# Performance work log

Hardware: AMD Instinct MI355X
Metric: run time of the kernel (lower is better)

The kernel has to match this reference:

```python
import jax, jax.numpy as jnp
import numpy as np

N_SRC, N_TGT, E = 50000, 10000, 150000
D_IN, D_OUT = 512, 512
N_ETYPES, N_NTYPES = 8, 4


def setup_inputs() -> dict:
    key = jax.random.key(0)
    ks = jax.random.split(key, 9)
    scale = 1.0 / np.sqrt(D_IN)
    return {
        "x_src": jax.random.normal(ks[0], (N_SRC, D_IN), jnp.float32),
        "x_target": jax.random.normal(ks[1], (N_TGT, D_IN), jnp.float32),
        "rel_W": jax.random.normal(ks[2], (N_ETYPES, D_IN, D_OUT), jnp.float32) * scale,
        "root_W": jax.random.normal(ks[3], (N_NTYPES, D_IN, D_OUT), jnp.float32) * scale,
        "root_b": jax.random.normal(ks[4], (N_NTYPES, D_OUT), jnp.float32) * scale,
        "edge_src": jax.random.randint(ks[5], (E,), 0, N_SRC, jnp.int64).astype(jnp.int32),
        "edge_dst": jax.random.randint(ks[6], (E,), 0, N_TGT, jnp.int64).astype(jnp.int32),
        "edge_type": jax.random.randint(ks[7], (E,), 0, N_ETYPES, jnp.int64).astype(jnp.int32),
        "target_node_type": jax.random.randint(ks[8], (N_TGT,), 0, N_NTYPES, jnp.int64).astype(jnp.int32),
    }


def reference(x_src, x_target, rel_W, root_W, root_b,
              edge_src, edge_dst, edge_type, target_node_type):
    T = rel_W.shape[0]
    n_tgt = x_target.shape[0]
    # Transform every source node under every relation (grouped GEMM),
    # then gather per edge: msg_e = W_{etype_e} @ x_src[src_e].
    h = jnp.einsum('ni,tio->tno', x_src, rel_W)          # [T, N_src, D_out]
    msg = h[edge_type, edge_src]                          # [E, D_out]
    # PyG aggr='mean' is applied per edge type then SUMMED across types:
    # segment-mean keyed by (dst, etype), empty segments contribute 0.
    seg = edge_dst * T + edge_type                        # [E]
    sums = jax.ops.segment_sum(msg, seg, num_segments=n_tgt * T)
    counts = jax.ops.segment_sum(jnp.ones((msg.shape[0],), msg.dtype), seg,
                                 num_segments=n_tgt * T)
    means = sums / jnp.maximum(counts, 1.0)[:, None]      # [N_tgt*T, D_out]
    out = means.reshape(n_tgt, T, -1).sum(axis=1)         # [N_tgt, D_out]
    # Per-node-type root linear (with bias), selected per target node.
    root = jnp.einsum('ni,tio->nto', x_target, root_W) + root_b[None]  # [N_tgt, NT, D_out]
    root_sel = jnp.take_along_axis(root, target_node_type[:, None, None], axis=1)[:, 0]
    return out + root_sel
```

## Files before the change

### kernel.cpp

```cpp
#include <hip/hip_runtime.h>
#include <hip/hip_bf16.h>

#define D 512
#define T_ETYPES 8
#define NT_TYPES 4
#define K_MAIN 4096
#define K_TOT 6144
#define SPLITS 4
#define KSPLIT 1536

typedef __attribute__((ext_vector_type(8))) short bf16x8;
typedef __attribute__((ext_vector_type(4))) float f32x4;

__device__ __forceinline__ unsigned short f2bf(float f) {
    union { float f; unsigned u; } u{f};
    unsigned r = u.u + 0x7FFF + ((u.u >> 16) & 1);
    return (unsigned short)(r >> 16);
}
__device__ __forceinline__ float bf2f(unsigned short h) {
    union { unsigned u; float f; } v{(unsigned)h << 16};
    return v.f;
}

__device__ __forceinline__ void gl16(const unsigned short* g, unsigned short* l) {
    __builtin_amdgcn_global_load_lds(
        (const __attribute__((address_space(1))) unsigned int*)g,
        (__attribute__((address_space(3))) unsigned int*)l,
        16, 0, 0);
}

__global__ void convert_weights(const float* __restrict__ relW,
                                const float* __restrict__ rootW,
                                unsigned short* __restrict__ WbT) {
    __shared__ float tile[32][33];
    int c0 = blockIdx.x * 32;
    int o0 = blockIdx.y * 32;
    int tid = threadIdx.x;
#pragma unroll
    for (int it = 0; it < 4; ++it) {
        int idx = it * 256 + tid;
        int oc = idx & 31, cc = idx >> 5;
        int c = c0 + cc, o = o0 + oc;
        float v = (c < K_MAIN) ? relW[(size_t)c * D + o]
                               : rootW[(size_t)(c - K_MAIN) * D + o];
        tile[cc][oc] = v;
    }
    __syncthreads();
#pragma unroll
    for (int it = 0; it < 4; ++it) {
        int idx = it * 256 + tid;
        int cc = idx & 31, oc = idx >> 5;
        WbT[(size_t)(o0 + oc) * K_TOT + (c0 + cc)] = f2bf(tile[cc][oc]);
    }
}

__global__ void hist_kernel(const int* __restrict__ edst, const int* __restrict__ etyp,
                            int* __restrict__ counts, int E) {
    int e = blockIdx.x * 256 + threadIdx.x;
    if (e < E) atomicAdd(&counts[edst[e] * T_ETYPES + etyp[e]], 1);
}

__global__ void scan1(const int* __restrict__ counts, int* __restrict__ partial,
                      int* __restrict__ blockSums, int n) {
    __shared__ int sh[256];
    int tid = threadIdx.x, i = blockIdx.x * 256 + tid;
    int c = (i < n) ? counts[i] : 0;
    int val = c;
    sh[tid] = val; __syncthreads();
#pragma unroll
    for (int off = 1; off < 256; off <<= 1) {
        int add = (tid >= off) ? sh[tid - off] : 0;
        __syncthreads();
        val += add; sh[tid] = val;
        __syncthreads();
    }
    if (i < n) partial[i] = val - c;
    if (tid == 255) blockSums[blockIdx.x] = val;
}

__global__ void scan2(int* __restrict__ blockSums, int nb) {
    __shared__ int sh[512];
    int tid = threadIdx.x;
    int c = (tid < nb) ? blockSums[tid] : 0;
    int val = c;
    sh[tid] = val; __syncthreads();
#pragma unroll
    for (int off = 1; off < 512; off <<= 1) {
        int add = (tid >= off) ? sh[tid - off] : 0;
        __syncthreads();
        val += add; sh[tid] = val;
        __syncthreads();
    }
    if (tid < nb) blockSums[tid] = val - c;
}

__global__ void scan3(const int* __restrict__ partial, const int* __restrict__ blockSums,
                      int* __restrict__ offsets, int* __restrict__ cursors, int n) {
    int i = blockIdx.x * 256 + threadIdx.x;
    if (i < n) {
        int v = partial[i] + blockSums[i >> 8];
        offsets[i] = v;
        cursors[i] = v;
    }
}

__global__ void scatter_kernel(const int* __restrict__ esrc, const int* __restrict__ edst,
                               const int* __restrict__ etyp, int* __restrict__ cursors,
                               int* __restrict__ perm, int E) {
    int e = blockIdx.x * 256 + threadIdx.x;
    if (e < E) {
        int seg = edst[e] * T_ETYPES + etyp[e];
        int pos = atomicAdd(&cursors[seg], 1);
        perm[pos] = esrc[e];
    }
}

__global__ void segmean(const float* __restrict__ x_src, const int* __restrict__ perm,
                        const int* __restrict__ offsets, const int* __restrict__ counts,
                        unsigned short* __restrict__ A, int nseg) {
    int seg = blockIdx.x * 4 + (threadIdx.x >> 6);
    if (seg >= nseg) return;
    int lane = threadIdx.x & 63;
    int beg = offsets[seg], cnt = counts[seg];
    float4 a0 = make_float4(0.f, 0.f, 0.f, 0.f);
    float4 a1 = make_float4(0.f, 0.f, 0.f, 0.f);
    for (int i = 0; i < cnt; ++i) {
        int s = perm[beg + i];
        const float4* p = reinterpret_cast<const float4*>(x_src + (size_t)s * D);
        float4 v0 = p[lane * 2], v1 = p[lane * 2 + 1];
        a0.x += v0.x; a0.y += v0.y; a0.z += v0.z; a0.w += v0.w;
        a1.x += v1.x; a1.y += v1.y; a1.z += v1.z; a1.w += v1.w;
    }
    float sc = (cnt > 0) ? 1.0f / (float)cnt : 0.0f;
    uint4 u;
    u.x = (unsigned)f2bf(a0.x * sc) | ((unsigned)f2bf(a0.y * sc) << 16);
    u.y = (unsigned)f2bf(a0.z * sc) | ((unsigned)f2bf(a0.w * sc) << 16);
    u.z = (unsigned)f2bf(a1.x * sc) | ((unsigned)f2bf(a1.y * sc) << 16);
    u.w = (unsigned)f2bf(a1.z * sc) | ((unsigned)f2bf(a1.w * sc) << 16);
    int dst = seg >> 3, t = seg & 7;
    *reinterpret_cast<uint4*>(A + (size_t)dst * K_TOT + t * D + lane * 8) = u;
}

__global__ void rootfill(const float* __restrict__ x_target, const int* __restrict__ tnt,
                         unsigned short* __restrict__ A, int M) {
    int n = blockIdx.x;
    int tid = threadIdx.x;
    int nt = tnt[n];
    int col = tid * 8;
    int g = col >> 9;
    uint4 u = make_uint4(0, 0, 0, 0);
    if (g == nt) {
        const float4* p = reinterpret_cast<const float4*>(x_target + (size_t)n * D + (col & 511));
        float4 v0 = p[0], v1 = p[1];
        u.x = (unsigned)f2bf(v0.x) | ((unsigned)f2bf(v0.y) << 16);
        u.y = (unsigned)f2bf(v0.z) | ((unsigned)f2bf(v0.w) << 16);
        u.z = (unsigned)f2bf(v1.x) | ((unsigned)f2bf(v1.y) << 16);
        u.w = (unsigned)f2bf(v1.z) | ((unsigned)f2bf(v1.w) << 16);
    }
    *reinterpret_cast<uint4*>(A + (size_t)n * K_TOT + K_MAIN + col) = u;
}

__global__ __launch_bounds__(256, 4)
void rgcn_gemm_sk(const unsigned short* __restrict__ A,
                  const unsigned short* __restrict__ WbT,
                  unsigned short* __restrict__ pbuf, int M, int MB) {
    __shared__ unsigned short As[128 * 32];
    __shared__ unsigned short Bs[128 * 32];
    const int tid = threadIdx.x;

    int d = blockIdx.x;
    int l = d;
    if ((gridDim.x & 7) == 0) {
        int cpx = gridDim.x >> 3;
        l = (d & 7) * cpx + (d >> 3);
    }
    const int nIdx = l & 3;
    const int mz = l >> 2;
    const int mIdx = mz % MB;
    const int zIdx = mz / MB;

    const int blockM = mIdx * 128;
    const int blockN = nIdx * 128;
    const int kBase = zIdx * KSPLIT;
    const int wid = tid >> 6, lane = tid & 63;
    const int wr = wid >> 1, wc = wid & 1;
    const int lr = lane & 15, lg = lane >> 4;

    f32x4 acc[4][4] = {};

    const int c0 = tid, c1 = 256 + tid;
    const unsigned short* Abase = A + (size_t)blockM * K_TOT + kBase;
    const unsigned short* Bbase = WbT + (size_t)blockN * K_TOT + kBase;

    for (int k0 = 0; k0 < KSPLIT; k0 += 32) {
        gl16(Abase + (size_t)(c0 >> 2) * K_TOT + k0 + (c0 & 3) * 8, &As[c0 * 8]);
        gl16(Abase + (size_t)(c1 >> 2) * K_TOT + k0 + (c1 & 3) * 8, &As[c1 * 8]);
        gl16(Bbase + (size_t)(c0 >> 2) * K_TOT + k0 + (c0 & 3) * 8, &Bs[c0 * 8]);
        gl16(Bbase + (size_t)(c1 >> 2) * K_TOT + k0 + (c1 & 3) * 8, &Bs[c1 * 8]);
        __syncthreads();

        bf16x8 a_frag[4], b_frag[4];
#pragma unroll
        for (int mi = 0; mi < 4; ++mi)
            a_frag[mi] = *reinterpret_cast<const bf16x8*>(&As[(wr * 64 + mi * 16 + lr) * 32 + lg * 8]);
#pragma unroll
        for (int ni = 0; ni < 4; ++ni)
            b_frag[ni] = *reinterpret_cast<const bf16x8*>(&Bs[(wc * 64 + ni * 16 + lr) * 32 + lg * 8]);
#pragma unroll
        for (int mi = 0; mi < 4; ++mi)
#pragma unroll
            for (int ni = 0; ni < 4; ++ni)
                acc[mi][ni] = __builtin_amdgcn_mfma_f32_16x16x32_bf16(a_frag[mi], b_frag[ni], acc[mi][ni], 0, 0, 0);
        __syncthreads();
    }

#pragma unroll
    for (int mi = 0; mi < 4; ++mi) {
#pragma unroll
        for (int r = 0; r < 4; ++r) {
            int row = blockM + wr * 64 + mi * 16 + lg * 4 + r;
            if (row < M) {
#pragma unroll
                for (int ni = 0; ni < 4; ++ni) {
                    int col = blockN + wc * 64 + ni * 16 + lr;
                    pbuf[((size_t)zIdx * M + row) * D + col] = f2bf(acc[mi][ni][r]);
                }
            }
        }
    }
}

__global__ void reduce_bias(const unsigned short* __restrict__ pbuf,
                            const int* __restrict__ tnt, const float* __restrict__ root_b,
                            float* __restrict__ out, int M) {
    int idx = blockIdx.x * 256 + threadIdx.x;
    if (idx >= M * (D / 8)) return;
    int row = idx >> 6;
    int col = (idx & 63) * 8;
    float s[8] = {0.f, 0.f, 0.f, 0.f, 0.f, 0.f, 0.f, 0.f};
#pragma unroll
    for (int sp = 0; sp < SPLITS; ++sp) {
        uint4 v = *reinterpret_cast<const uint4*>(pbuf + ((size_t)sp * M + row) * D + col);
        unsigned u[4] = {v.x, v.y, v.z, v.w};
#pragma unroll
        for (int j = 0; j < 4; ++j) {
            s[2 * j]     += bf2f((unsigned short)(u[j] & 0xFFFF));
            s[2 * j + 1] += bf2f((unsigned short)(u[j] >> 16));
        }
    }
    const float* b = root_b + (size_t)tnt[row] * D + col;
    float4 o0, o1;
    o0.x = s[0] + b[0]; o0.y = s[1] + b[1]; o0.z = s[2] + b[2]; o0.w = s[3] + b[3];
    o1.x = s[4] + b[4]; o1.y = s[5] + b[5]; o1.z = s[6] + b[6]; o1.w = s[7] + b[7];
    float* o = out + (size_t)row * D + col;
    *reinterpret_cast<float4*>(o) = o0;
    *reinterpret_cast<float4*>(o + 4) = o1;
}

extern "C" void kernel_launch(void* const* d_in, const int* in_sizes, int n_in,
                              void* d_out, int out_size, void* d_ws, size_t ws_size,
                              hipStream_t stream) {
    const float* x_src    = (const float*)d_in[0];
    const float* x_target = (const float*)d_in[1];
    const float* relW     = (const float*)d_in[2];
    const float* rootW    = (const float*)d_in[3];
    const float* rootb    = (const float*)d_in[4];
    const int*   esrc     = (const int*)d_in[5];
    const int*   edst     = (const int*)d_in[6];
    const int*   etyp     = (const int*)d_in[7];
    const int*   tnt      = (const int*)d_in[8];
    float* out = (float*)d_out;

    const int E = in_sizes[5];
    const int M = in_sizes[8];
    const int NSEG = M * T_ETYPES;
    const int NB = (NSEG + 255) / 256;
    const int MB = (M + 127) / 128;

    char* ws = (char*)d_ws;
    size_t off = 0;
    unsigned short* Abf = (unsigned short*)(ws + off); off += (size_t)M * K_TOT * 2;
    unsigned short* WbT = (unsigned short*)(ws + off); off += (size_t)D * K_TOT * 2;
    unsigned short* pb  = (unsigned short*)(ws + off); off += (size_t)SPLITS * M * D * 2;
    int* counts    = (int*)(ws + off); off += (size_t)NSEG * 4;
    int* partial   = (int*)(ws + off); off += (size_t)NSEG * 4;
    int* offsets   = (int*)(ws + off); off += (size_t)NSEG * 4;
    int* cursors   = (int*)(ws + off); off += (size_t)NSEG * 4;
    int* blockSums = (int*)(ws + off); off += 512 * 4;
    int* perm      = (int*)(ws + off); off += (size_t)E * 4;

    hipMemsetAsync(counts, 0, (size_t)NSEG * 4, stream);

    convert_weights<<<dim3(K_TOT / 32, D / 32), 256, 0, stream>>>(relW, rootW, WbT);
    hist_kernel<<<(E + 255) / 256, 256, 0, stream>>>(edst, etyp, counts, E);
    scan1<<<NB, 256, 0, stream>>>(counts, partial, blockSums, NSEG);
    scan2<<<1, 512, 0, stream>>>(blockSums, NB);
    scan3<<<NB, 256, 0, stream>>>(partial, blockSums, offsets, cursors, NSEG);
    scatter_kernel<<<(E + 255) / 256, 256, 0, stream>>>(esrc, edst, etyp, cursors, perm, E);
    segmean<<<(NSEG + 3) / 4, 256, 0, stream>>>(x_src, perm, offsets, counts, Abf, NSEG);
    rootfill<<<M, 256, 0, stream>>>(x_target, tnt, Abf, M);
    rgcn_gemm_sk<<<MB * 4 * SPLITS, 256, 0, stream>>>(Abf, WbT, pb, M, MB);
    reduce_bias<<<(M * (D / 8) + 255) / 256, 256, 0, stream>>>(pb, tnt, rootb, out, M);
}
```

Before: 206.8 us.

## Group target rows by node type to shrink root GEMM K dimension

Target rows are sorted by node type into 128-row-aligned groups, so each GEMM tile needs only its own type's 512 root-weight columns instead of all 2048 zero-padded ones. The A matrix shrinks from 6144 to 4608 columns and the split-K count is retuned to six splits of 768. This removes the multiply-by-zero work and the zero-fill writes, at the cost of extra histogram/scatter kernels, permuted writes, padding rows, and more partial buffers for the reduction. Padded rows in A are never written, but those outputs are masked.

```diff
diff --git a/kernel.cpp b/kernel.cpp
--- a/kernel.cpp
+++ b/kernel.cpp
@@ -5,9 +5,10 @@
 #define T_ETYPES 8
 #define NT_TYPES 4
 #define K_MAIN 4096
-#define K_TOT 6144
-#define SPLITS 4
-#define KSPLIT 1536
+#define K_A 4608
+#define K_B 6144
+#define SPLITS 6
+#define KSPLIT 768
 
 typedef __attribute__((ext_vector_type(8))) short bf16x8;
 typedef __attribute__((ext_vector_type(4))) float f32x4;
@@ -50,7 +51,7 @@
     for (int it = 0; it < 4; ++it) {
         int idx = it * 256 + tid;
         int cc = idx & 31, oc = idx >> 5;
-        WbT[(size_t)(o0 + oc) * K_TOT + (c0 + cc)] = f2bf(tile[cc][oc]);
+        WbT[(size_t)(o0 + oc) * K_B + (c0 + cc)] = f2bf(tile[cc][oc]);
     }
 }
 
@@ -115,8 +116,42 @@
     }
 }
 
+__global__ void thist(const int* __restrict__ tnt, int* __restrict__ tcnt, int M) {
+    __shared__ int h[NT_TYPES];
+    if (threadIdx.x < NT_TYPES) h[threadIdx.x] = 0;
+    __syncthreads();
+    int i = blockIdx.x * 256 + threadIdx.x;
+    if (i < M) atomicAdd(&h[tnt[i]], 1);
+    __syncthreads();
+    if (threadIdx.x < NT_TYPES) atomicAdd(&tcnt[threadIdx.x], h[threadIdx.x]);
+}
+
+__global__ void tprep(const int* __restrict__ tcnt, int* __restrict__ gstart,
+                      int* __restrict__ endv, int* __restrict__ tcur) {
+    if (threadIdx.x == 0 && blockIdx.x == 0) {
+        int s = 0;
+        for (int g = 0; g < NT_TYPES; ++g) {
+            gstart[g] = s; tcur[g] = s; endv[g] = s + tcnt[g];
+            s += ((tcnt[g] + 127) >> 7) << 7;
+        }
+        gstart[NT_TYPES] = s;
+    }
+}
+
+__global__ void tscatter(const int* __restrict__ tnt, int* __restrict__ tcur,
+                         int* __restrict__ rowperm, int* __restrict__ invperm, int M) {
+    int n = blockIdx.x * 256 + threadIdx.x;
+    if (n < M) {
+        int g = tnt[n];
+        int p = atomicAdd(&tcur[g], 1);
+        rowperm[p] = n;
+        invperm[n] = p;
+    }
+}
+
 __global__ void segmean(const float* __restrict__ x_src, const int* __restrict__ perm,
                         const int* __restrict__ offsets, const int* __restrict__ counts,
+                        const int* __restrict__ invperm,
                         unsigned short* __restrict__ A, int nseg) {
     int seg = blockIdx.x * 4 + (threadIdx.x >> 6);
     if (seg >= nseg) return;
@@ -138,32 +173,32 @@
     u.z = (unsigned)f2bf(a1.x * sc) | ((unsigned)f2bf(a1.y * sc) << 16);
     u.w = (unsigned)f2bf(a1.z * sc) | ((unsigned)f2bf(a1.w * sc) << 16);
     int dst = seg >> 3, t = seg & 7;
-    *reinterpret_cast<uint4*>(A + (size_t)dst * K_TOT + t * D + lane * 8) = u;
-}
-
-__global__ void rootfill(const float* __restrict__ x_target, const int* __restrict__ tnt,
+    int nrow = invperm[dst];
+    *reinterpret_cast<uint4*>(A + (size_t)nrow * K_A + t * D + lane * 8) = u;
+}
+
+__global__ void rootfill(const float* __restrict__ x_target, const int* __restrict__ invperm,
                          unsigned short* __restrict__ A, int M) {
-    int n = blockIdx.x;
-    int tid = threadIdx.x;
-    int nt = tnt[n];
-    int col = tid * 8;
-    int g = col >> 9;
-    uint4 u = make_uint4(0, 0, 0, 0);
-    if (g == nt) {
-        const float4* p = reinterpret_cast<const float4*>(x_target + (size_t)n * D + (col & 511));
-        float4 v0 = p[0], v1 = p[1];
-        u.x = (unsigned)f2bf(v0.x) | ((unsigned)f2bf(v0.y) << 16);
-        u.y = (unsigned)f2bf(v0.z) | ((unsigned)f2bf(v0.w) << 16);
-        u.z = (unsigned)f2bf(v1.x) | ((unsigned)f2bf(v1.y) << 16);
-        u.w = (unsigned)f2bf(v1.z) | ((unsigned)f2bf(v1.w) << 16);
-    }
-    *reinterpret_cast<uint4*>(A + (size_t)n * K_TOT + K_MAIN + col) = u;
+    int idx = blockIdx.x * 256 + threadIdx.x;
+    if (idx >= M * 64) return;
+    int n = idx >> 6;
+    int col = (idx & 63) * 8;
+    const float4* p = reinterpret_cast<const float4*>(x_target + (size_t)n * D + col);
+    float4 v0 = p[0], v1 = p[1];
+    uint4 u;
+    u.x = (unsigned)f2bf(v0.x) | ((unsigned)f2bf(v0.y) << 16);
+    u.y = (unsigned)f2bf(v0.z) | ((unsigned)f2bf(v0.w) << 16);
+    u.z = (unsigned)f2bf(v1.x) | ((unsigned)f2bf(v1.y) << 16);
+    u.w = (unsigned)f2bf(v1.z) | ((unsigned)f2bf(v1.w) << 16);
+    *reinterpret_cast<uint4*>(A + (size_t)invperm[n] * K_A + K_MAIN + col) = u;
 }
 
 __global__ __launch_bounds__(256, 4)
 void rgcn_gemm_sk(const unsigned short* __restrict__ A,
                   const unsigned short* __restrict__ WbT,
-                  unsigned short* __restrict__ pbuf, int M, int MB) {
+                  unsigned short* __restrict__ pbuf,
+                  const int* __restrict__ gstart, const int* __restrict__ endv,
+                  int MBP, int MPc) {
     __shared__ unsigned short As[128 * 32];
     __shared__ unsigned short Bs[128 * 32];
     const int tid = threadIdx.x;
@@ -176,12 +211,16 @@
     }
     const int nIdx = l & 3;
     const int mz = l >> 2;
-    const int mIdx = mz % MB;
-    const int zIdx = mz / MB;
+    const int mIdx = mz % MBP;
+    const int zIdx = mz / MBP;
 
     const int blockM = mIdx * 128;
     const int blockN = nIdx * 128;
     const int kBase = zIdx * KSPLIT;
+    const int g = (blockM >= gstart[1]) + (blockM >= gstart[2]) + (blockM >= gstart[3]);
+    const int endRow = endv[g];
+    const int rootOff = g * 512;
+
     const int wid = tid >> 6, lane = tid & 63;
     const int wr = wid >> 1, wc = wid & 1;
     const int lr = lane & 15, lg = lane >> 4;
@@ -189,14 +228,17 @@
     f32x4 acc[4][4] = {};
 
     const int c0 = tid, c1 = 256 + tid;
-    const unsigned short* Abase = A + (size_t)blockM * K_TOT + kBase;
-    const unsigned short* Bbase = WbT + (size_t)blockN * K_TOT + kBase;
-
-    for (int k0 = 0; k0 < KSPLIT; k0 += 32) {
-        gl16(Abase + (size_t)(c0 >> 2) * K_TOT + k0 + (c0 & 3) * 8, &As[c0 * 8]);
-        gl16(Abase + (size_t)(c1 >> 2) * K_TOT + k0 + (c1 & 3) * 8, &As[c1 * 8]);
-        gl16(Bbase + (size_t)(c0 >> 2) * K_TOT + k0 + (c0 & 3) * 8, &Bs[c0 * 8]);
-        gl16(Bbase + (size_t)(c1 >> 2) * K_TOT + k0 + (c1 & 3) * 8, &Bs[c1 * 8]);
+    const unsigned short* Abase = A + (size_t)blockM * K_A + kBase;
+    const unsigned short* Bbase = WbT + (size_t)blockN * K_B;
+
+    for (int t = 0; t < KSPLIT / 32; ++t) {
+        const int k0 = t * 32;
+        const int kc = kBase + k0;
+        const int bc = (kc < K_MAIN) ? kc : kc + rootOff;
+        gl16(Abase + (size_t)(c0 >> 2) * K_A + k0 + (c0 & 3) * 8, &As[c0 * 8]);
+        gl16(Abase + (size_t)(c1 >> 2) * K_A + k0 + (c1 & 3) * 8, &As[c1 * 8]);
+        gl16(Bbase + (size_t)(c0 >> 2) * K_B + bc + (c0 & 3) * 8, &Bs[c0 * 8]);
+        gl16(Bbase + (size_t)(c1 >> 2) * K_B + bc + (c1 & 3) * 8, &Bs[c1 * 8]);
         __syncthreads();
 
         bf16x8 a_frag[4], b_frag[4];
@@ -219,11 +261,11 @@
 #pragma unroll
         for (int r = 0; r < 4; ++r) {
             int row = blockM + wr * 64 + mi * 16 + lg * 4 + r;
-            if (row < M) {
+            if (row < endRow) {
 #pragma unroll
                 for (int ni = 0; ni < 4; ++ni) {
                     int col = blockN + wc * 64 + ni * 16 + lr;
-                    pbuf[((size_t)zIdx * M + row) * D + col] = f2bf(acc[mi][ni][r]);
+                    pbuf[((size_t)zIdx * MPc + row) * D + col] = f2bf(acc[mi][ni][r]);
                 }
             }
         }
@@ -231,16 +273,19 @@
 }
 
 __global__ void reduce_bias(const unsigned short* __restrict__ pbuf,
-                            const int* __restrict__ tnt, const float* __restrict__ root_b,
-                            float* __restrict__ out, int M) {
+                            const int* __restrict__ rowperm, const int* __restrict__ tnt,
+                            const float* __restrict__ root_b,
+                            float* __restrict__ out, int MPc) {
     int idx = blockIdx.x * 256 + threadIdx.x;
-    if (idx >= M * (D / 8)) return;
-    int row = idx >> 6;
+    if (idx >= MPc * 64) return;
+    int nrow = idx >> 6;
     int col = (idx & 63) * 8;
+    int orig = rowperm[nrow];
+    if (orig < 0) return;
     float s[8] = {0.f, 0.f, 0.f, 0.f, 0.f, 0.f, 0.f, 0.f};
 #pragma unroll
     for (int sp = 0; sp < SPLITS; ++sp) {
-        uint4 v = *reinterpret_cast<const uint4*>(pbuf + ((size_t)sp * M + row) * D + col);
+        uint4 v = *reinterpret_cast<const uint4*>(pbuf + ((size_t)sp * MPc + nrow) * D + col);
         unsigned u[4] = {v.x, v.y, v.z, v.w};
 #pragma unroll
         for (int j = 0; j < 4; ++j) {
@@ -248,11 +293,11 @@
             s[2 * j + 1] += bf2f((unsigned short)(u[j] >> 16));
         }
     }
-    const float* b = root_b + (size_t)tnt[row] * D + col;
+    const float* b = root_b + (size_t)tnt[orig] * D + col;
     float4 o0, o1;
     o0.x = s[0] + b[0]; o0.y = s[1] + b[1]; o0.z = s[2] + b[2]; o0.w = s[3] + b[3];
     o1.x = s[4] + b[4]; o1.y = s[5] + b[5]; o1.z = s[6] + b[6]; o1.w = s[7] + b[7];
-    float* o = out + (size_t)row * D + col;
+    float* o = out + (size_t)orig * D + col;
     *reinterpret_cast<float4*>(o) = o0;
     *reinterpret_cast<float4*>(o + 4) = o1;
 }
@@ -275,30 +320,41 @@
     const int M = in_sizes[8];
     const int NSEG = M * T_ETYPES;
     const int NB = (NSEG + 255) / 256;
-    const int MB = (M + 127) / 128;
+    const int MBP = (M + 127) / 128 + (NT_TYPES - 1);
+    const int MPc = MBP * 128;
 
     char* ws = (char*)d_ws;
     size_t off = 0;
-    unsigned short* Abf = (unsigned short*)(ws + off); off += (size_t)M * K_TOT * 2;
-    unsigned short* WbT = (unsigned short*)(ws + off); off += (size_t)D * K_TOT * 2;
-    unsigned short* pb  = (unsigned short*)(ws + off); off += (size_t)SPLITS * M * D * 2;
+    unsigned short* Abf = (unsigned short*)(ws + off); off += (size_t)MPc * K_A * 2;
+    unsigned short* WbT = (unsigned short*)(ws + off); off += (size_t)D * K_B * 2;
+    unsigned short* pb  = (unsigned short*)(ws + off); off += (size_t)SPLITS * MPc * D * 2;
     int* counts    = (int*)(ws + off); off += (size_t)NSEG * 4;
+    int* tcnt      = (int*)(ws + off); off += NT_TYPES * 4;
     int* partial   = (int*)(ws + off); off += (size_t)NSEG * 4;
     int* offsets   = (int*)(ws + off); off += (size_t)NSEG * 4;
     int* cursors   = (int*)(ws + off); off += (size_t)NSEG * 4;
     int* blockSums = (int*)(ws + off); off += 512 * 4;
     int* perm      = (int*)(ws + off); off += (size_t)E * 4;
-
-    hipMemsetAsync(counts, 0, (size_t)NSEG * 4, stream);
-
-    convert_weights<<<dim3(K_TOT / 32, D / 32), 256, 0, stream>>>(relW, rootW, WbT);
+    int* gstart    = (int*)(ws + off); off += 8 * 4;
+    int* endv      = (int*)(ws + off); off += 8 * 4;
+    int* tcur      = (int*)(ws + off); off += 8 * 4;
+    int* rowperm   = (int*)(ws + off); off += (size_t)MPc * 4;
+    int* invperm   = (int*)(ws + off); off += (size_t)M * 4;
+
+    hipMemsetAsync(counts, 0, ((size_t)NSEG + NT_TYPES) * 4, stream);
+    hipMemsetAsync(rowperm, 0xFF, (size_t)MPc * 4, stream);
+
+    convert_weights<<<dim3(K_B / 32, D / 32), 256, 0, stream>>>(relW, rootW, WbT);
+    thist<<<(M + 255) / 256, 256, 0, stream>>>(tnt, tcnt, M);
+    tprep<<<1, 64, 0, stream>>>(tcnt, gstart, endv, tcur);
+    tscatter<<<(M + 255) / 256, 256, 0, stream>>>(tnt, tcur, rowperm, invperm, M);
     hist_kernel<<<(E + 255) / 256, 256, 0, stream>>>(edst, etyp, counts, E);
     scan1<<<NB, 256, 0, stream>>>(counts, partial, blockSums, NSEG);
     scan2<<<1, 512, 0, stream>>>(blockSums, NB);
     scan3<<<NB, 256, 0, stream>>>(partial, blockSums, offsets, cursors, NSEG);
     scatter_kernel<<<(E + 255) / 256, 256, 0, stream>>>(esrc, edst, etyp, cursors, perm, E);
-    segmean<<<(NSEG + 3) / 4, 256, 0, stream>>>(x_src, perm, offsets, counts, Abf, NSEG);
-    rootfill<<<M, 256, 0, stream>>>(x_target, tnt, Abf, M);
-    rgcn_gemm_sk<<<MB * 4 * SPLITS, 256, 0, stream>>>(Abf, WbT, pb, M, MB);
-    reduce_bias<<<(M * (D / 8) + 255) / 256, 256, 0, stream>>>(pb, tnt, rootb, out, M);
-}
+    segmean<<<(NSEG + 3) / 4, 256, 0, stream>>>(x_src, perm, offsets, counts, invperm, Abf, NSEG);
+    rootfill<<<(M * 64 + 255) / 256, 256, 0, stream>>>(x_target, invperm, Abf, M);
+    rgcn_gemm_sk<<<MBP * 4 * SPLITS, 256, 0, stream>>>(Abf, WbT, pb, gstart, endv, MBP, MPc);
+    reduce_bias<<<(MPc * 64 + 255) / 256, 256, 0, stream>>>(pb, rowperm, tnt, rootb, out, MPc);
+}
```

Measured after the change: 248.6 us. 1.2x slower.
